# Performance work log

Measured on AMD Instinct MI355X. Metric: run time of the kernel, lower is better.

The kernel has to match this reference:

```python
import jax, jax.numpy as jnp
import numpy as np

W_WIDTH = 2048   # neurons per topological batch
N_BATCH = 9      # number of non-input topological batches
NUM_IN = W_WIDTH # input neurons


def setup_inputs() -> dict:
    key = jax.random.key(0)
    k_x, k_w, k_b = jax.random.split(key, 3)
    scale = 1.0 / jnp.sqrt(jnp.float32(W_WIDTH))
    x = jax.random.normal(k_x, (W_WIDTH,), dtype=jnp.float32)
    weights = jax.random.normal(k_w, (N_BATCH, W_WIDTH, W_WIDTH), dtype=jnp.float32) * scale
    bias = jax.random.normal(k_b, (N_BATCH * W_WIDTH,), dtype=jnp.float32) * 0.01
    masks = jnp.ones((N_BATCH, W_WIDTH, W_WIDTH), dtype=bool)
    # idx for topo batch i = ids of previous layer = [i*W, (i+1)*W)
    idxs = jnp.arange(N_BATCH * W_WIDTH, dtype=jnp.int64 if jax.config.jax_enable_x64 else jnp.int32).reshape(N_BATCH, W_WIDTH)
    return {"x": x, "weights": weights, "bias": bias, "masks": masks, "idxs": idxs}


def reference(x, weights, bias, masks, idxs):
    W = x.shape[0]
    L = weights.shape[0]
    num_neurons = (L + 1) * W
    # dropout_p = 0 -> dropout_keep is all ones; input neurons get x directly
    values = jnp.zeros((num_neurons,), dtype=x.dtype).at[:W].set(x)
    for i in range(L):  # fixed small loop over topological batches
        gathered = values[idxs[i]]                                   # gather [W]
        eff_w = weights[i] * masks[i].astype(x.dtype)                # masked weights [W, W]
        affine = eff_w @ gathered + bias[i * W:(i + 1) * W]          # affine [W]
        # hidden batches use silu; the final batch is the output neurons (identity elem act)
        out = jax.nn.silu(affine) if i < L - 1 else affine
        values = values.at[(i + 1) * W:(i + 2) * W].set(out)         # scatter
    # output_activation_group = identity
    return values[L * W:]
```

## Files before the change

### kernel.cpp

```cpp
#include <hip/hip_runtime.h>


#define W_WIDTH  2048
#define TPB      512
#define N_WAVES  (TPB / 64)
#define NBLOCKS  (W_WIDTH / N_WAVES)
#define N_LAYERS 9

typedef float    v4f __attribute__((ext_vector_type(4)));
typedef unsigned v4u __attribute__((ext_vector_type(4)));

__device__ __forceinline__ void issue_weights(const float* wrow_lane,
                                              v4f* wn, float* br,
                                              const float* bptr)
{
    const float* b0 = wrow_lane;
    const float* b1 = wrow_lane + 1024;
    asm volatile("global_load_dwordx4 %0, %1, off nt"             : "=v"(wn[0]) : "v"(b0) : "memory");
    asm volatile("global_load_dwordx4 %0, %1, off offset:1024 nt" : "=v"(wn[1]) : "v"(b0) : "memory");
    asm volatile("global_load_dwordx4 %0, %1, off offset:2048 nt" : "=v"(wn[2]) : "v"(b0) : "memory");
    asm volatile("global_load_dwordx4 %0, %1, off offset:3072 nt" : "=v"(wn[3]) : "v"(b0) : "memory");
    asm volatile("global_load_dwordx4 %0, %1, off nt"             : "=v"(wn[4]) : "v"(b1) : "memory");
    asm volatile("global_load_dwordx4 %0, %1, off offset:1024 nt" : "=v"(wn[5]) : "v"(b1) : "memory");
    asm volatile("global_load_dwordx4 %0, %1, off offset:2048 nt" : "=v"(wn[6]) : "v"(b1) : "memory");
    asm volatile("global_load_dwordx4 %0, %1, off offset:3072 nt" : "=v"(wn[7]) : "v"(b1) : "memory");
    asm volatile("global_load_dword %0, %1, off"                  : "=v"(*br)   : "v"(bptr) : "memory");
}

__global__ __launch_bounds__(TPB)
void mlp_fused(const float* __restrict__ x,
               const float* __restrict__ wgt,
               const float* __restrict__ bias,
               float*       __restrict__ out,
               unsigned*    __restrict__ rec)
{
    __shared__ __align__(16) float xs[W_WIDTH];
    __shared__ float arow[N_WAVES];
    const int tid  = threadIdx.x;
    const int lane = tid & 63;
    const int wv   = tid >> 6;
    const int row  = blockIdx.x * N_WAVES + wv;

    v4f   wbuf[2][8];
    float br[2];

    issue_weights(wgt + (size_t)row * W_WIDTH + lane * 4, wbuf[0], &br[0],
                  bias + row);
    v4f x4;
    {
        const float* ap = x + 4 * tid;
        asm volatile("global_load_dwordx4 %0, %1, off" : "=v"(x4) : "v"(ap) : "memory");
    }
    asm volatile("s_waitcnt vmcnt(0)" ::: "memory");
    __builtin_amdgcn_sched_barrier(0);
    *(v4f*)&xs[4 * tid] = x4;
    __syncthreads();

    #pragma unroll
    for (int i = 0; i < N_LAYERS; ++i) {
        if (i < N_LAYERS - 1)
            issue_weights(wgt + ((size_t)(i + 1) * W_WIDTH + row) * W_WIDTH + lane * 4,
                          wbuf[(i + 1) & 1], &br[(i + 1) & 1],
                          bias + (size_t)(i + 1) * W_WIDTH + row);

        float acc = 0.f;
        const v4f* xv = (const v4f*)xs;
        #pragma unroll
        for (int k = 0; k < 8; ++k) {
            v4f wk = wbuf[i & 1][k];
            v4f xk = xv[k * 64 + lane];
            acc = fmaf(wk.x, xk.x, acc);
            acc = fmaf(wk.y, xk.y, acc);
            acc = fmaf(wk.z, xk.z, acc);
            acc = fmaf(wk.w, xk.w, acc);
        }
        #pragma unroll
        for (int off = 32; off > 0; off >>= 1)
            acc += __shfl_xor(acc, off, 64);
        float a = acc + br[i & 1];

        if (i == N_LAYERS - 1) {
            if (lane == 0) out[row] = a;
        } else {
            if (lane == 0) arow[wv] = a / (1.f + __expf(-a));
            asm volatile("s_waitcnt lgkmcnt(0)" ::: "memory");
            __builtin_amdgcn_s_barrier();

            const unsigned stamp = (unsigned)(i + 1);
            unsigned* rbase = rec + ((i & 1) ? 4096 : 0);

            if (wv == 0 && lane < 4) {
                v4u pkt;
                pkt.x = __float_as_uint(arow[2 * lane]);
                pkt.y = __float_as_uint(arow[2 * lane + 1]);
                pkt.z = stamp;
                pkt.w = 0u;
                unsigned* sp = rbase + ((size_t)blockIdx.x * 4 + lane) * 4;
                asm volatile("global_store_dwordx4 %0, %1, off sc0 sc1"
                             :: "v"(sp), "v"(pkt) : "memory");
            }

            const unsigned* p0 = rbase + (size_t)(2 * tid) * 4;
            const unsigned* p1 = rbase + (size_t)(2 * tid + 1) * 4;
            v4u f0, f1;
            for (;;) {
                asm volatile("global_load_dwordx4 %0, %1, off sc0 sc1"
                             : "=v"(f0) : "v"(p0) : "memory");
                asm volatile("global_load_dwordx4 %0, %1, off sc0 sc1"
                             : "=v"(f1) : "v"(p1) : "memory");
                asm volatile("s_waitcnt vmcnt(0)" ::: "memory");
                __builtin_amdgcn_sched_barrier(0);
                bool ok = (f0.z == stamp) && (f1.z == stamp);
                if (__all(ok)) break;
                __builtin_amdgcn_s_sleep(1);
            }

            v4f nx;
            nx.x = __uint_as_float(f0.x);
            nx.y = __uint_as_float(f0.y);
            nx.z = __uint_as_float(f1.x);
            nx.w = __uint_as_float(f1.y);
            *(v4f*)&xs[4 * tid] = nx;
            asm volatile("s_waitcnt lgkmcnt(0)" ::: "memory");
            __builtin_amdgcn_s_barrier();
        }
    }
}

extern "C" void kernel_launch(void* const* d_in, const int* in_sizes, int n_in,
                              void* d_out, int out_size, void* d_ws, size_t ws_size,
                              hipStream_t stream)
{
    (void)in_sizes; (void)n_in; (void)out_size; (void)ws_size;

    const float* x    = (const float*)d_in[0];
    const float* wgt  = (const float*)d_in[1];
    const float* bias = (const float*)d_in[2];
    float*       out  = (float*)d_out;

    unsigned* rec = (unsigned*)d_ws;

    hipMemsetAsync(rec, 0, 32768, stream);

    mlp_fused<<<dim3(NBLOCKS), dim3(TPB), 0, stream>>>(
        x, wgt, bias, out, rec);
}
```

Before: 279.3 us.

## Stage weights into LDS via async loads and add dedicated communication wave

```diff
diff --git a/kernel.cpp b/kernel.cpp
--- a/kernel.cpp
+++ b/kernel.cpp
@@ -2,29 +2,32 @@
 
 
 #define W_WIDTH  2048
-#define TPB      512
-#define N_WAVES  (TPB / 64)
-#define NBLOCKS  (W_WIDTH / N_WAVES)
+#define NCW      8
+#define TPB      ((NCW + 1) * 64)
+#define NBLOCKS  (W_WIDTH / NCW)
 #define N_LAYERS 9
 
 typedef float    v4f __attribute__((ext_vector_type(4)));
 typedef unsigned v4u __attribute__((ext_vector_type(4)));
 
-__device__ __forceinline__ void issue_weights(const float* wrow_lane,
-                                              v4f* wn, float* br,
-                                              const float* bptr)
+typedef const __attribute__((address_space(1))) void GAS;
+typedef __attribute__((address_space(3))) void       LAS;
+
+__device__ __forceinline__ void fenced_barrier()
 {
-    const float* b0 = wrow_lane;
-    const float* b1 = wrow_lane + 1024;
-    asm volatile("global_load_dwordx4 %0, %1, off nt"             : "=v"(wn[0]) : "v"(b0) : "memory");
-    asm volatile("global_load_dwordx4 %0, %1, off offset:1024 nt" : "=v"(wn[1]) : "v"(b0) : "memory");
-    asm volatile("global_load_dwordx4 %0, %1, off offset:2048 nt" : "=v"(wn[2]) : "v"(b0) : "memory");
-    asm volatile("global_load_dwordx4 %0, %1, off offset:3072 nt" : "=v"(wn[3]) : "v"(b0) : "memory");
-    asm volatile("global_load_dwordx4 %0, %1, off nt"             : "=v"(wn[4]) : "v"(b1) : "memory");
-    asm volatile("global_load_dwordx4 %0, %1, off offset:1024 nt" : "=v"(wn[5]) : "v"(b1) : "memory");
-    asm volatile("global_load_dwordx4 %0, %1, off offset:2048 nt" : "=v"(wn[6]) : "v"(b1) : "memory");
-    asm volatile("global_load_dwordx4 %0, %1, off offset:3072 nt" : "=v"(wn[7]) : "v"(b1) : "memory");
-    asm volatile("global_load_dword %0, %1, off"                  : "=v"(*br)   : "v"(bptr) : "memory");
+    __builtin_amdgcn_sched_barrier(0);
+    asm volatile("" ::: "memory");
+    __builtin_amdgcn_s_barrier();
+    asm volatile("" ::: "memory");
+    __builtin_amdgcn_sched_barrier(0);
+}
+
+__device__ __forceinline__ void stage_row(const float* grow_lane, float* lrow)
+{
+    #pragma unroll
+    for (int k = 0; k < 8; ++k)
+        __builtin_amdgcn_global_load_lds((GAS*)(grow_lane + k * 256),
+                                         (LAS*)(lrow + k * 256), 16, 0, 0);
 }
 
 __global__ __launch_bounds__(TPB)
@@ -34,96 +37,109 @@
                float*       __restrict__ out,
                unsigned*    __restrict__ rec)
 {
+    __shared__ __align__(16) float lds_w[2][NCW][W_WIDTH];
     __shared__ __align__(16) float xs[W_WIDTH];
-    __shared__ float arow[N_WAVES];
-    const int tid  = threadIdx.x;
-    const int lane = tid & 63;
-    const int wv   = tid >> 6;
-    const int row  = blockIdx.x * N_WAVES + wv;
+    __shared__ float arow[NCW];
 
-    v4f   wbuf[2][8];
-    float br[2];
+    const int  tid  = threadIdx.x;
+    const int  lane = tid & 63;
+    const int  wv   = tid >> 6;
+    const bool comp = (wv < NCW);
+    const int  row  = blockIdx.x * NCW + wv;
 
-    issue_weights(wgt + (size_t)row * W_WIDTH + lane * 4, wbuf[0], &br[0],
-                  bias + row);
-    v4f x4;
-    {
-        const float* ap = x + 4 * tid;
-        asm volatile("global_load_dwordx4 %0, %1, off" : "=v"(x4) : "v"(ap) : "memory");
+    float b_r[N_LAYERS];
+
+    if (comp) {
+        #pragma unroll
+        for (int j = 0; j < N_LAYERS; ++j)
+            b_r[j] = bias[j * W_WIDTH + row];
+        v4f x4 = *(const v4f*)(x + 4 * tid);
+        *(v4f*)&xs[4 * tid] = x4;
+        stage_row(wgt + (size_t)row * W_WIDTH + lane * 4, lds_w[0][wv]);
     }
-    asm volatile("s_waitcnt vmcnt(0)" ::: "memory");
-    __builtin_amdgcn_sched_barrier(0);
-    *(v4f*)&xs[4 * tid] = x4;
     __syncthreads();
 
     #pragma unroll
     for (int i = 0; i < N_LAYERS; ++i) {
-        if (i < N_LAYERS - 1)
-            issue_weights(wgt + ((size_t)(i + 1) * W_WIDTH + row) * W_WIDTH + lane * 4,
-                          wbuf[(i + 1) & 1], &br[(i + 1) & 1],
-                          bias + (size_t)(i + 1) * W_WIDTH + row);
+        if (comp) {
+            if (i < N_LAYERS - 1) {
+                stage_row(wgt + ((size_t)(i + 1) * W_WIDTH + row) * W_WIDTH + lane * 4,
+                          lds_w[(i + 1) & 1][wv]);
+                asm volatile("s_waitcnt vmcnt(8)" ::: "memory");
+            } else {
+                asm volatile("s_waitcnt vmcnt(0)" ::: "memory");
+            }
+            __builtin_amdgcn_sched_barrier(0);
 
-        float acc = 0.f;
-        const v4f* xv = (const v4f*)xs;
-        #pragma unroll
-        for (int k = 0; k < 8; ++k) {
-            v4f wk = wbuf[i & 1][k];
-            v4f xk = xv[k * 64 + lane];
-            acc = fmaf(wk.x, xk.x, acc);
-            acc = fmaf(wk.y, xk.y, acc);
-            acc = fmaf(wk.z, xk.z, acc);
-            acc = fmaf(wk.w, xk.w, acc);
+            float acc = 0.f;
+            const v4f* wr = (const v4f*)lds_w[i & 1][wv];
+            const v4f* xv = (const v4f*)xs;
+            #pragma unroll
+            for (int k = 0; k < 8; ++k) {
+                v4f wk = wr[k * 64 + lane];
+                v4f xk = xv[k * 64 + lane];
+                acc = fmaf(wk.x, xk.x, acc);
+                acc = fmaf(wk.y, xk.y, acc);
+                acc = fmaf(wk.z, xk.z, acc);
+                acc = fmaf(wk.w, xk.w, acc);
+            }
+            #pragma unroll
+            for (int off = 32; off > 0; off >>= 1)
+                acc += __shfl_xor(acc, off, 64);
+            float a = acc + b_r[i];
+
+            if (i == N_LAYERS - 1) {
+                if (lane == 0) out[row] = a;
+            } else if (lane == 0) {
+                arow[wv] = a / (1.f + __expf(-a));
+            }
         }
-        #pragma unroll
-        for (int off = 32; off > 0; off >>= 1)
-            acc += __shfl_xor(acc, off, 64);
-        float a = acc + br[i & 1];
+        if (i == N_LAYERS - 1) break;
 
-        if (i == N_LAYERS - 1) {
-            if (lane == 0) out[row] = a;
-        } else {
-            if (lane == 0) arow[wv] = a / (1.f + __expf(-a));
-            asm volatile("s_waitcnt lgkmcnt(0)" ::: "memory");
-            __builtin_amdgcn_s_barrier();
+        asm volatile("s_waitcnt lgkmcnt(0)" ::: "memory");
+        fenced_barrier();
 
-            const unsigned stamp = (unsigned)(i + 1);
-            unsigned* rbase = rec + ((i & 1) ? 4096 : 0);
+        const unsigned stamp = (unsigned)(i + 1);
+        unsigned* rb = rec + ((i & 1) ? 4096 : 0);
 
-            if (wv == 0 && lane < 4) {
+        if (!comp) {
+            if (lane < 4) {
                 v4u pkt;
                 pkt.x = __float_as_uint(arow[2 * lane]);
                 pkt.y = __float_as_uint(arow[2 * lane + 1]);
                 pkt.z = stamp;
                 pkt.w = 0u;
-                unsigned* sp = rbase + ((size_t)blockIdx.x * 4 + lane) * 4;
+                unsigned* sp = rb + ((size_t)blockIdx.x * 4 + lane) * 4;
                 asm volatile("global_store_dwordx4 %0, %1, off sc0 sc1"
                              :: "v"(sp), "v"(pkt) : "memory");
             }
 
-            const unsigned* p0 = rbase + (size_t)(2 * tid) * 4;
-            const unsigned* p1 = rbase + (size_t)(2 * tid + 1) * 4;
-            v4u f0, f1;
             for (;;) {
-                asm volatile("global_load_dwordx4 %0, %1, off sc0 sc1"
-                             : "=v"(f0) : "v"(p0) : "memory");
-                asm volatile("global_load_dwordx4 %0, %1, off sc0 sc1"
-                             : "=v"(f1) : "v"(p1) : "memory");
-                asm volatile("s_waitcnt vmcnt(0)" ::: "memory");
-                __builtin_amdgcn_sched_barrier(0);
-                bool ok = (f0.z == stamp) && (f1.z == stamp);
+                bool ok = true;
+                #pragma unroll
+                for (int j = 0; j < 16; ++j) {
+                    const unsigned* sp = rb + (size_t)(j * 64 + lane) * 4 + 2;
+                    unsigned s = __hip_atomic_load(sp, __ATOMIC_RELAXED,
+                                                   __HIP_MEMORY_SCOPE_AGENT);
+                    ok = ok && (s == stamp);
+                }
                 if (__all(ok)) break;
                 __builtin_amdgcn_s_sleep(1);
             }
 
-            v4f nx;
-            nx.x = __uint_as_float(f0.x);
-            nx.y = __uint_as_float(f0.y);
-            nx.z = __uint_as_float(f1.x);
-            nx.w = __uint_as_float(f1.y);
-            *(v4f*)&xs[4 * tid] = nx;
+            #pragma unroll
+            for (int j = 0; j < 16; ++j) {
+                const unsigned* cp = rb + (size_t)(j * 64 + lane) * 4;
+                unsigned u0 = __hip_atomic_load(cp + 0, __ATOMIC_RELAXED,
+                                                __HIP_MEMORY_SCOPE_AGENT);
+                unsigned u1 = __hip_atomic_load(cp + 1, __ATOMIC_RELAXED,
+                                                __HIP_MEMORY_SCOPE_AGENT);
+                xs[128 * j + 2 * lane]     = __uint_as_float(u0);
+                xs[128 * j + 2 * lane + 1] = __uint_as_float(u1);
+            }
             asm volatile("s_waitcnt lgkmcnt(0)" ::: "memory");
-            __builtin_amdgcn_s_barrier();
         }
+        fenced_barrier();
     }
 }
 
```

Result: slower. 304.8 us (+9.1%).
